# Kernel tuning notes

Hardware: AMD Instinct MI355X
Metric: run time of the kernel (lower is better)

The kernel has to match this reference:

```python
import jax, jax.numpy as jnp
import numpy as np
import math

CS = 8       # cell_size
NBINS = 8
SIGMA = 1.0
IMG = 224
BATCH = 256
TWO_PI = 2.0 * math.pi


def setup_inputs() -> dict:
    key = jax.random.key(0)
    x = jax.random.normal(key, (BATCH, 3, IMG, IMG), dtype=jnp.float32)
    coords = jnp.arange(CS, dtype=jnp.float32) - (CS - 1) / 2.0
    xx, yy = jnp.meshgrid(coords, coords, indexing='ij')
    gauss = jnp.exp(-(xx ** 2 + yy ** 2) / (2.0 * SIGMA ** 2)).reshape(1, CS * CS)
    kx = jnp.array([[-1., 0., 1.], [-2., 0., 2.], [-1., 0., 1.]], dtype=jnp.float32).reshape(1, 1, 3, 3)
    ky = jnp.array([[-1., -2., -1.], [0., 0., 0.], [1., 2., 1.]], dtype=jnp.float32).reshape(1, 1, 3, 3)
    return {"x": x, "gauss": gauss, "kx": kx, "ky": ky}


def _conv(im, k):
    # NCHW conv, padding=1, stride=1 (matches F.conv2d(..., padding=1))
    return jax.lax.conv_general_dilated(
        im, k, window_strides=(1, 1), padding=[(1, 1), (1, 1)],
        dimension_numbers=('NCHW', 'OIHW', 'NCHW'))


def reference(x, gauss, kx, ky):
    bs, _, H, W = x.shape
    gray = 0.2989 * x[:, 0:1] + 0.587 * x[:, 1:2] + 0.114 * x[:, 2:3]  # [bs,1,H,W]
    gx = _conv(gray, kx)
    gy = _conv(gray, ky)
    mag = jnp.sqrt(gx ** 2 + gy ** 2 + 1e-6)
    ang = jnp.mod(jnp.arctan2(gy, gx), TWO_PI)
    Hc, Wc = H // CS, W // CS
    n_cells = Hc * Wc

    def to_cells(a):
        # [bs,1,H,W] -> [bs*n_cells, CS*CS], within-cell order (kh,kw) row-major
        # matching F.unfold's kernel-position ordering.
        return a.reshape(bs, Hc, CS, Wc, CS).transpose(0, 1, 3, 2, 4).reshape(bs * n_cells, CS * CS)

    mags = to_cells(mag) * gauss  # gauss broadcasts over kernel positions
    angs = to_cells(ang)

    bin_w = TWO_PI / NBINS
    idx = (angs / bin_w).astype(jnp.int32) % NBINS  # [bs*n_cells, CS*CS]

    N = bs * n_cells
    hist = jnp.zeros((N, NBINS), dtype=mags.dtype)
    hist = hist.at[jnp.arange(N)[:, None], idx].add(mags)  # scatter_add per cell
    hist = hist.reshape(bs, n_cells * NBINS)
    hist = hist / (jnp.linalg.norm(hist, axis=1, keepdims=True) + 1e-6)
    return hist
```

## Files before the change

kernel.cpp:

```cpp
#include <hip/hip_runtime.h>
#include <math.h>

#define NBINS 8
#define IMG 224
#define HC 28
#define OUTPER (HC*HC*NBINS)
#define BATCH 256
#define PL4 12544
#define WROWS 10
#define WSTRIDE 232
#define GOFF 4

__global__ __launch_bounds__(256) void hog_main_kernel(
    const float4* __restrict__ x, const float* __restrict__ gauss,
    float* __restrict__ out, float* __restrict__ partial)
{
    __shared__ float g[4][WROWS][WSTRIDE];
    const int tid  = threadIdx.x;
    const int wv   = tid >> 6;
    const int lane = tid & 63;
    const int gw   = blockIdx.x * 4 + wv;
    const int b    = gw / HC;
    const int cr   = gw - b * HC;
    const int r0   = cr * 8;

    const float4* xb = x + (size_t)b * 3 * PL4;

    if (lane < WROWS * 2) {
        int rr = lane >> 1, cc = (lane & 1) ? (GOFF + IMG) : (GOFF - 1);
        g[wv][rr][cc] = 0.f;
    }

    #pragma unroll 3
    for (int k = 0; k < 9; ++k) {
        int idx = k * 64 + lane;
        bool act = idx < 560;
        int ii = act ? idx : 559;
        int row = ii / 56, c4 = ii - row * 56;
        int gr = r0 - 1 + row;
        int grc = gr < 0 ? 0 : (gr > IMG - 1 ? IMG - 1 : gr);
        const float4* p = xb + grc * 56 + c4;
        float4 R = p[0];
        float4 G = p[PL4];
        float4 B = p[2 * PL4];
        bool z = (gr < 0) || (gr > IMG - 1);
        float4 v;
        v.x = z ? 0.f : 0.2989f * R.x + 0.587f * G.x + 0.114f * B.x;
        v.y = z ? 0.f : 0.2989f * R.y + 0.587f * G.y + 0.114f * B.y;
        v.z = z ? 0.f : 0.2989f * R.z + 0.587f * G.z + 0.114f * B.z;
        v.w = z ? 0.f : 0.2989f * R.w + 0.587f * G.w + 0.114f * B.w;
        if (act) *(float4*)&g[wv][row][GOFF + 4 * c4] = v;
    }
    __builtin_amdgcn_wave_barrier();

    const int wc = lane & 7;
    float wgt[8];
    #pragma unroll
    for (int i = 0; i < 8; ++i) wgt[i] = gauss[i * 8 + wc];

    float ssq = 0.f;
    const size_t obase = (size_t)b * OUTPER + (size_t)cr * IMG;

    for (int ch = 0; ch < 4; ++ch) {
        int c = ch * 64 + lane;
        bool act = c < IMG;
        int cc = act ? c : IMG - 1;

        float h[8];
        #pragma unroll
        for (int k2 = 0; k2 < 8; ++k2) h[k2] = 0.f;

        float t0 = g[wv][0][cc + 3], t1 = g[wv][0][cc + 4], t2 = g[wv][0][cc + 5];
        float m0 = g[wv][1][cc + 3], m1 = g[wv][1][cc + 4], m2 = g[wv][1][cc + 5];

        #pragma unroll
        for (int sr = 0; sr < 8; ++sr) {
            float b0 = g[wv][sr + 2][cc + 3], b1 = g[wv][sr + 2][cc + 4],
                  b2 = g[wv][sr + 2][cc + 5];
            float gx = (t2 - t0) + 2.f * (m2 - m0) + (b2 - b0);
            float gy = (b0 - t0) + 2.f * (b1 - t1) + (b2 - t2);
            float mag = sqrtf(gx * gx + gy * gy + 1e-6f);
            float ax = fabsf(gx), ay = fabsf(gy);

            int bin;
            if (gy > 0.f)       bin = (gx > 0.f)  ? ((gy < gx) ? 0 : 1)
                                    : (gx == 0.f) ? 2 : ((ay > ax) ? 2 : 3);
            else if (gy == 0.f) bin = (gx < 0.f) ? 4 : 0;
            else                bin = (gx < 0.f)  ? ((ay < ax) ? 4 : 5)
                                    : (gx == 0.f) ? 6 : ((ay > ax) ? 6 : 7);

            float wm = wgt[sr] * mag;
            #pragma unroll
            for (int k2 = 0; k2 < 8; ++k2) h[k2] += (bin == k2) ? wm : 0.f;

            t0 = m0; t1 = m1; t2 = m2;
            m0 = b0; m1 = b1; m2 = b2;
        }

        #pragma unroll
        for (int sh = 1; sh < 8; sh <<= 1) {
            #pragma unroll
            for (int k2 = 0; k2 < 8; ++k2) h[k2] += __shfl_xor(h[k2], sh, 64);
        }
        float v = (wc < 4) ? ((wc < 2) ? (wc == 0 ? h[0] : h[1])
                                      : (wc == 2 ? h[2] : h[3]))
                           : ((wc < 6) ? (wc == 4 ? h[4] : h[5])
                                      : (wc == 6 ? h[6] : h[7]));
        if (act) {
            out[obase + c] = v;
            ssq += v * v;
        }
    }

    #pragma unroll
    for (int o = 32; o > 0; o >>= 1) ssq += __shfl_down(ssq, o, 64);
    if (lane == 0) partial[gw] = ssq;
}

__global__ __launch_bounds__(512) void hog_norm_kernel(
    float* __restrict__ out, const float* __restrict__ partial)
{
    const int b = blockIdx.x;
    __shared__ float s_inv;
    if (threadIdx.x < 64) {
        float s = (threadIdx.x < HC) ? partial[b * HC + threadIdx.x] : 0.f;
        #pragma unroll
        for (int o = 16; o > 0; o >>= 1) s += __shfl_down(s, o, 64);
        if (threadIdx.x == 0) s_inv = 1.0f / (sqrtf(s) + 1e-6f);
    }
    __syncthreads();
    float inv = s_inv;
    float4* o4 = (float4*)(out + (size_t)b * OUTPER);
    for (int i = threadIdx.x; i < OUTPER / 4; i += 512) {
        float4 v = o4[i];
        v.x *= inv; v.y *= inv; v.z *= inv; v.w *= inv;
        o4[i] = v;
    }
}

extern "C" void kernel_launch(void* const* d_in, const int* in_sizes, int n_in,
                              void* d_out, int out_size, void* d_ws, size_t ws_size,
                              hipStream_t stream) {
    const float* x     = (const float*)d_in[0];
    const float* gauss = (const float*)d_in[1];
    float* out     = (float*)d_out;
    float* partial = (float*)d_ws;

    hog_main_kernel<<<BATCH * HC / 4, 256, 0, stream>>>(
        (const float4*)x, gauss, out, partial);
    hog_norm_kernel<<<BATCH, 512, 0, stream>>>(out, partial);
}
```

Before: 252.8 us.

## Replace LDS staging with register-resident rows and cross-lane shuffles per column chunk

```diff
diff --git a/kernel.cpp b/kernel.cpp
--- a/kernel.cpp
+++ b/kernel.cpp
@@ -6,135 +6,148 @@
 #define HC 28
 #define OUTPER (HC*HC*NBINS)
 #define BATCH 256
-#define PL4 12544
-#define WROWS 10
-#define WSTRIDE 232
-#define GOFF 4
+#define PL (IMG*IMG)
 
 __global__ __launch_bounds__(256) void hog_main_kernel(
-    const float4* __restrict__ x, const float* __restrict__ gauss,
+    const float* __restrict__ x, const float* __restrict__ gauss,
     float* __restrict__ out, float* __restrict__ partial)
 {
-    __shared__ float g[4][WROWS][WSTRIDE];
     const int tid  = threadIdx.x;
     const int wv   = tid >> 6;
     const int lane = tid & 63;
-    const int gw   = blockIdx.x * 4 + wv;
-    const int b    = gw / HC;
-    const int cr   = gw - b * HC;
+    const int bc   = blockIdx.x;
+    const int b    = bc / HC;
+    const int cr   = bc - b * HC;
     const int r0   = cr * 8;
+    const int c0   = wv * 64;
+    const int c    = c0 + lane;
+    const int cl   = c > IMG - 1 ? IMG - 1 : c;
 
-    const float4* xb = x + (size_t)b * 3 * PL4;
+    const float* xb = x + (size_t)b * 3 * PL;
 
-    if (lane < WROWS * 2) {
-        int rr = lane >> 1, cc = (lane & 1) ? (GOFF + IMG) : (GOFF - 1);
-        g[wv][rr][cc] = 0.f;
+    float v[10];
+    #pragma unroll
+    for (int j = 0; j < 10; ++j) {
+        int gr  = r0 - 1 + j;
+        int grc = gr < 0 ? 0 : (gr > IMG - 1 ? IMG - 1 : gr);
+        const float* p = xb + grc * IMG + cl;
+        float R = p[0], G = p[PL], B = p[2 * PL];
+        float gv = 0.2989f * R + 0.587f * G + 0.114f * B;
+        v[j] = (gr < 0 || gr > IMG - 1) ? 0.f : gv;
     }
 
-    #pragma unroll 3
-    for (int k = 0; k < 9; ++k) {
-        int idx = k * 64 + lane;
-        bool act = idx < 560;
-        int ii = act ? idx : 559;
-        int row = ii / 56, c4 = ii - row * 56;
-        int gr = r0 - 1 + row;
+    float hl, hr;
+    {
+        int jl = lane - 54; jl = jl < 0 ? 0 : (jl > 9 ? 9 : jl);
+        int gr = r0 - 1 + jl;
         int grc = gr < 0 ? 0 : (gr > IMG - 1 ? IMG - 1 : gr);
-        const float4* p = xb + grc * 56 + c4;
-        float4 R = p[0];
-        float4 G = p[PL4];
-        float4 B = p[2 * PL4];
-        bool z = (gr < 0) || (gr > IMG - 1);
-        float4 v;
-        v.x = z ? 0.f : 0.2989f * R.x + 0.587f * G.x + 0.114f * B.x;
-        v.y = z ? 0.f : 0.2989f * R.y + 0.587f * G.y + 0.114f * B.y;
-        v.z = z ? 0.f : 0.2989f * R.z + 0.587f * G.z + 0.114f * B.z;
-        v.w = z ? 0.f : 0.2989f * R.w + 0.587f * G.w + 0.114f * B.w;
-        if (act) *(float4*)&g[wv][row][GOFF + 4 * c4] = v;
+        int colL = c0 - 1; bool zc = colL < 0; int colc = zc ? 0 : colL;
+        const float* p = xb + grc * IMG + colc;
+        float R = p[0], G = p[PL], B = p[2 * PL];
+        float gv = 0.2989f * R + 0.587f * G + 0.114f * B;
+        hl = (zc || gr < 0 || gr > IMG - 1) ? 0.f : gv;
     }
-    __builtin_amdgcn_wave_barrier();
+    {
+        int jr = lane - 44; jr = jr < 0 ? 0 : (jr > 9 ? 9 : jr);
+        int gr = r0 - 1 + jr;
+        int grc = gr < 0 ? 0 : (gr > IMG - 1 ? IMG - 1 : gr);
+        int colR = c0 + 64; bool zc = colR > IMG - 1; int colc = zc ? IMG - 1 : colR;
+        const float* p = xb + grc * IMG + colc;
+        float R = p[0], G = p[PL], B = p[2 * PL];
+        float gv = 0.2989f * R + 0.587f * G + 0.114f * B;
+        hr = (zc || gr < 0 || gr > IMG - 1) ? 0.f : gv;
+    }
 
     const int wc = lane & 7;
     float wgt[8];
     #pragma unroll
     for (int i = 0; i < 8; ++i) wgt[i] = gauss[i * 8 + wc];
 
+    auto mklr = [&](int j, float& lf, float& rt) {
+        float a = __shfl_up(v[j], 1, 64);
+        float hLj = __shfl(hl, 54 + j, 64);
+        lf = (lane == 0) ? hLj : a;
+        float d = __shfl_down(v[j], 1, 64);
+        float hRj = __shfl(hr, 44 + j, 64);
+        d = (lane == 63) ? hRj : d;
+        rt = (c >= IMG - 1) ? 0.f : d;
+    };
+
+    float h[8];
+    #pragma unroll
+    for (int k = 0; k < 8; ++k) h[k] = 0.f;
+
+    float tL, tC, tR, mL, mC, mR;
+    mklr(0, tL, tR); tC = v[0];
+    mklr(1, mL, mR); mC = v[1];
+
+    #pragma unroll
+    for (int sr = 0; sr < 8; ++sr) {
+        float bL, bR, bC = v[sr + 2];
+        mklr(sr + 2, bL, bR);
+
+        float gx = (tR - tL) + 2.f * (mR - mL) + (bR - bL);
+        float gy = (bL - tL) + 2.f * (bC - tC) + (bR - tR);
+        float mag = sqrtf(gx * gx + gy * gy + 1e-6f);
+        float ax = fabsf(gx), ay = fabsf(gy);
+
+        int bin;
+        if (gy > 0.f)       bin = (gx > 0.f)  ? ((gy < gx) ? 0 : 1)
+                                : (gx == 0.f) ? 2 : ((ay > ax) ? 2 : 3);
+        else if (gy == 0.f) bin = (gx < 0.f) ? 4 : 0;
+        else                bin = (gx < 0.f)  ? ((ay < ax) ? 4 : 5)
+                                : (gx == 0.f) ? 6 : ((ay > ax) ? 6 : 7);
+
+        float wm = wgt[sr] * mag;
+        #pragma unroll
+        for (int k = 0; k < 8; ++k) h[k] += (bin == k) ? wm : 0.f;
+
+        tL = mL; tC = mC; tR = mR;
+        mL = bL; mC = bC; mR = bR;
+    }
+
+    #pragma unroll
+    for (int sh = 1; sh < 8; sh <<= 1) {
+        #pragma unroll
+        for (int k = 0; k < 8; ++k) h[k] += __shfl_xor(h[k], sh, 64);
+    }
+    float val = (wc < 4) ? ((wc < 2) ? (wc == 0 ? h[0] : h[1])
+                                    : (wc == 2 ? h[2] : h[3]))
+                         : ((wc < 6) ? (wc == 4 ? h[4] : h[5])
+                                    : (wc == 6 ? h[6] : h[7]));
     float ssq = 0.f;
-    const size_t obase = (size_t)b * OUTPER + (size_t)cr * IMG;
-
-    for (int ch = 0; ch < 4; ++ch) {
-        int c = ch * 64 + lane;
-        bool act = c < IMG;
-        int cc = act ? c : IMG - 1;
-
-        float h[8];
-        #pragma unroll
-        for (int k2 = 0; k2 < 8; ++k2) h[k2] = 0.f;
-
-        float t0 = g[wv][0][cc + 3], t1 = g[wv][0][cc + 4], t2 = g[wv][0][cc + 5];
-        float m0 = g[wv][1][cc + 3], m1 = g[wv][1][cc + 4], m2 = g[wv][1][cc + 5];
-
-        #pragma unroll
-        for (int sr = 0; sr < 8; ++sr) {
-            float b0 = g[wv][sr + 2][cc + 3], b1 = g[wv][sr + 2][cc + 4],
-                  b2 = g[wv][sr + 2][cc + 5];
-            float gx = (t2 - t0) + 2.f * (m2 - m0) + (b2 - b0);
-            float gy = (b0 - t0) + 2.f * (b1 - t1) + (b2 - t2);
-            float mag = sqrtf(gx * gx + gy * gy + 1e-6f);
-            float ax = fabsf(gx), ay = fabsf(gy);
-
-            int bin;
-            if (gy > 0.f)       bin = (gx > 0.f)  ? ((gy < gx) ? 0 : 1)
-                                    : (gx == 0.f) ? 2 : ((ay > ax) ? 2 : 3);
-            else if (gy == 0.f) bin = (gx < 0.f) ? 4 : 0;
-            else                bin = (gx < 0.f)  ? ((ay < ax) ? 4 : 5)
-                                    : (gx == 0.f) ? 6 : ((ay > ax) ? 6 : 7);
-
-            float wm = wgt[sr] * mag;
-            #pragma unroll
-            for (int k2 = 0; k2 < 8; ++k2) h[k2] += (bin == k2) ? wm : 0.f;
-
-            t0 = m0; t1 = m1; t2 = m2;
-            m0 = b0; m1 = b1; m2 = b2;
-        }
-
-        #pragma unroll
-        for (int sh = 1; sh < 8; sh <<= 1) {
-            #pragma unroll
-            for (int k2 = 0; k2 < 8; ++k2) h[k2] += __shfl_xor(h[k2], sh, 64);
-        }
-        float v = (wc < 4) ? ((wc < 2) ? (wc == 0 ? h[0] : h[1])
-                                      : (wc == 2 ? h[2] : h[3]))
-                           : ((wc < 6) ? (wc == 4 ? h[4] : h[5])
-                                      : (wc == 6 ? h[6] : h[7]));
-        if (act) {
-            out[obase + c] = v;
-            ssq += v * v;
-        }
+    if (c < IMG) {
+        out[(size_t)b * OUTPER + (size_t)cr * IMG + c] = val;
+        ssq = val * val;
     }
 
     #pragma unroll
     for (int o = 32; o > 0; o >>= 1) ssq += __shfl_down(ssq, o, 64);
-    if (lane == 0) partial[gw] = ssq;
+    if (lane == 0) partial[bc * 4 + wv] = ssq;
 }
 
-__global__ __launch_bounds__(512) void hog_norm_kernel(
+__global__ __launch_bounds__(256) void hog_norm_kernel(
     float* __restrict__ out, const float* __restrict__ partial)
 {
-    const int b = blockIdx.x;
+    const int b = blockIdx.x, tid = threadIdx.x;
+    __shared__ float wsum[4];
     __shared__ float s_inv;
-    if (threadIdx.x < 64) {
-        float s = (threadIdx.x < HC) ? partial[b * HC + threadIdx.x] : 0.f;
-        #pragma unroll
-        for (int o = 16; o > 0; o >>= 1) s += __shfl_down(s, o, 64);
-        if (threadIdx.x == 0) s_inv = 1.0f / (sqrtf(s) + 1e-6f);
+    float s = (tid < HC * 4) ? partial[b * HC * 4 + tid] : 0.f;
+    #pragma unroll
+    for (int o = 32; o > 0; o >>= 1) s += __shfl_down(s, o, 64);
+    if ((tid & 63) == 0) wsum[tid >> 6] = s;
+    __syncthreads();
+    if (tid == 0) {
+        float t = wsum[0] + wsum[1] + wsum[2] + wsum[3];
+        s_inv = 1.0f / (sqrtf(t) + 1e-6f);
     }
     __syncthreads();
     float inv = s_inv;
     float4* o4 = (float4*)(out + (size_t)b * OUTPER);
-    for (int i = threadIdx.x; i < OUTPER / 4; i += 512) {
-        float4 v = o4[i];
-        v.x *= inv; v.y *= inv; v.z *= inv; v.w *= inv;
-        o4[i] = v;
+    for (int i = tid; i < OUTPER / 4; i += 256) {
+        float4 w = o4[i];
+        w.x *= inv; w.y *= inv; w.z *= inv; w.w *= inv;
+        o4[i] = w;
     }
 }
 
@@ -146,7 +159,6 @@
     float* out     = (float*)d_out;
     float* partial = (float*)d_ws;
 
-    hog_main_kernel<<<BATCH * HC / 4, 256, 0, stream>>>(
-        (const float4*)x, gauss, out, partial);
-    hog_norm_kernel<<<BATCH, 512, 0, stream>>>(out, partial);
+    hog_main_kernel<<<BATCH * HC, 256, 0, stream>>>(x, gauss, out, partial);
+    hog_norm_kernel<<<BATCH, 256, 0, stream>>>(out, partial);
 }
```

After: 226.7 us. 1.12x faster.
